# Performance work log

Hardware: AMD Instinct MI355X
Metric: run time of the kernel (lower is better)

Reference implementation:

```python
import jax, jax.numpy as jnp
import numpy as np

N, E, IN, OUT, T = 50000, 800000, 16, 16, 8
LN_EPS = 1e-5


def setup_inputs() -> dict:
    key = jax.random.key(0)
    ks = jax.random.split(key, 8)
    x = jax.random.normal(ks[0], (N, IN), dtype=jnp.float32)
    edge_index = jax.random.randint(ks[1], (2, E), 0, N, dtype=jnp.int64)
    edge_attr = jax.random.normal(ks[2], (E, T), dtype=jnp.float32)
    # LayerNorm params
    ln_gamma = jnp.ones((IN,), dtype=jnp.float32)
    ln_beta = jnp.zeros((IN,), dtype=jnp.float32)
    # edge_nn: Linear(t, in*out)
    w_edge = jax.random.normal(ks[3], (T, IN * OUT), dtype=jnp.float32) * (1.0 / np.sqrt(T))
    b_edge = jax.random.normal(ks[4], (IN * OUT,), dtype=jnp.float32) * 0.01
    # NNConv root weight [in, out] and bias [out]
    root = jax.random.normal(ks[5], (IN, OUT), dtype=jnp.float32) * (1.0 / np.sqrt(IN))
    bias = jax.random.normal(ks[6], (OUT,), dtype=jnp.float32) * 0.01
    return {"x": x, "edge_index": edge_index, "edge_attr": edge_attr,
            "ln_gamma": ln_gamma, "ln_beta": ln_beta,
            "w_edge": w_edge, "b_edge": b_edge, "root": root, "bias": bias}


def reference(x, edge_index, edge_attr, ln_gamma, ln_beta, w_edge, b_edge, root, bias):
    # pre: LayerNorm -> ReLU (Dropout is identity in eval mode)
    mu = jnp.mean(x, axis=-1, keepdims=True)
    var = jnp.mean((x - mu) ** 2, axis=-1, keepdims=True)
    h = (x - mu) * jax.lax.rsqrt(var + LN_EPS) * ln_gamma + ln_beta
    h = jax.nn.relu(h)  # [N, IN]

    # edge MLP -> per-edge weight matrices [E, IN, OUT]
    theta = (edge_attr @ w_edge + b_edge).reshape(E, IN, OUT)

    src = edge_index[0]  # message source j
    dst = edge_index[1]  # aggregation target i (PyG source_to_target flow)

    # per-edge matmul: x_j [E, IN] x theta [E, IN, OUT] -> [E, OUT]
    msg = jnp.einsum('ei,eio->eo', h[src], theta)

    # scatter-add into target nodes
    agg = jax.ops.segment_sum(msg, dst, num_segments=N)  # [N, OUT]

    # root transform + bias
    out = agg + h @ root + bias
    return out
```

## Files before the change

### kernel.cpp

```cpp
#include <hip/hip_runtime.h>

#define N_NODES 50000
#define E_EDGES 800000
#define NTILES  (E_EDGES / 16)

typedef __attribute__((ext_vector_type(8))) short short8;
typedef __attribute__((ext_vector_type(4))) float floatx4;

__device__ __forceinline__ short f2bf(float x) {
    union { float f; unsigned u; } v; v.f = x;
    unsigned r = v.u + 0x7FFFu + ((v.u >> 16) & 1u);
    return (short)(r >> 16);
}

__global__ __launch_bounds__(256) void node_kernel(
    const float* __restrict__ x, const float* __restrict__ gamma,
    const float* __restrict__ beta, const float* __restrict__ root,
    const float* __restrict__ bias, float* __restrict__ h,
    float* __restrict__ out)
{
    int n = blockIdx.x * blockDim.x + threadIdx.x;
    if (n >= N_NODES) return;
    const float* xr = x + n * 16;
    float xv[16];
    #pragma unroll
    for (int i = 0; i < 4; ++i) ((floatx4*)xv)[i] = ((const floatx4*)xr)[i];
    float mu = 0.f;
    #pragma unroll
    for (int i = 0; i < 16; ++i) mu += xv[i];
    mu *= (1.f / 16.f);
    float var = 0.f;
    #pragma unroll
    for (int i = 0; i < 16; ++i) { float d = xv[i] - mu; var += d * d; }
    var *= (1.f / 16.f);
    float rs = rsqrtf(var + 1e-5f);
    float hv[16];
    #pragma unroll
    for (int i = 0; i < 16; ++i) {
        float t = (xv[i] - mu) * rs * gamma[i] + beta[i];
        hv[i] = t > 0.f ? t : 0.f;
    }
    float* hr = h + n * 16;
    #pragma unroll
    for (int i = 0; i < 4; ++i) ((floatx4*)hr)[i] = ((floatx4*)hv)[i];
    float ov[16];
    #pragma unroll
    for (int o = 0; o < 16; ++o) ov[o] = bias[o];
    #pragma unroll
    for (int i = 0; i < 16; ++i) {
        float hi = hv[i];
        #pragma unroll
        for (int o = 0; o < 16; ++o) ov[o] += hi * root[i * 16 + o];
    }
    float* orow = out + n * 16;
    #pragma unroll
    for (int i = 0; i < 4; ++i) ((floatx4*)orow)[i] = ((floatx4*)ov)[i];
}

__global__ __launch_bounds__(256) void edge_kernel(
    const int* __restrict__ eidx, const float* __restrict__ ea,
    const float* __restrict__ w_edge, const float* __restrict__ b_edge,
    const float* __restrict__ h, float* __restrict__ out)
{
    const int lane = threadIdx.x & 63;
    const int wid  = threadIdx.x >> 6;
    const int m = lane & 15;
    const int q = lane >> 4;

    short8 bfrag[5];
    #pragma unroll
    for (int c = 0; c < 5; ++c) {
        short8 f;
        #pragma unroll
        for (int j = 0; j < 8; ++j) {
            int k = 32 * c + 8 * q + j;
            float v = 0.f;
            if (k < 128)      v = w_edge[(k >> 4) * 256 + (k & 15) * 16 + m];
            else if (k < 144) v = b_edge[(k - 128) * 16 + m];
            f[j] = f2bf(v);
        }
        bfrag[c] = f;
    }

    const int nw = (gridDim.x * blockDim.x) >> 6;
    for (int tile = blockIdx.x * (blockDim.x >> 6) + wid; tile < NTILES; tile += nw) {
        const int e   = tile * 16 + m;
        const int src = eidx[e];
        const int dst = eidx[E_EDGES + e];

        const float* er = ea + (size_t)e * 8;
        floatx4 ea0 = ((const floatx4*)er)[0];
        floatx4 ea1 = ((const floatx4*)er)[1];

        const float* hr = h + src * 16 + 8 * (q & 1);
        floatx4 h0 = ((const floatx4*)hr)[0];
        floatx4 h1 = ((const floatx4*)hr)[1];
        float hh[8] = {h0.x, h0.y, h0.z, h0.w, h1.x, h1.y, h1.z, h1.w};

        floatx4 acc = {0.f, 0.f, 0.f, 0.f};
        const int hi_t = q >> 1;
        #pragma unroll
        for (int c = 0; c < 4; ++c) {
            float t_even, t_odd;
            if (c == 0)      { t_even = ea0.x; t_odd = ea0.y; }
            else if (c == 1) { t_even = ea0.z; t_odd = ea0.w; }
            else if (c == 2) { t_even = ea1.x; t_odd = ea1.y; }
            else             { t_even = ea1.z; t_odd = ea1.w; }
            float s = hi_t ? t_odd : t_even;
            short8 af;
            #pragma unroll
            for (int j = 0; j < 8; ++j) af[j] = f2bf(s * hh[j]);
            acc = __builtin_amdgcn_mfma_f32_16x16x32_bf16(af, bfrag[c], acc, 0, 0, 0);
        }
        short8 af4;
        #pragma unroll
        for (int j = 0; j < 8; ++j) af4[j] = (q < 2) ? f2bf(hh[j]) : (short)0;
        acc = __builtin_amdgcn_mfma_f32_16x16x32_bf16(af4, bfrag[4], acc, 0, 0, 0);

        #pragma unroll
        for (int r = 0; r < 4; ++r) {
            int dr = __shfl(dst, 4 * q + r, 64);
            atomicAdd(out + (size_t)dr * 16 + m, acc[r]);
        }
    }
}

extern "C" void kernel_launch(void* const* d_in, const int* in_sizes, int n_in,
                              void* d_out, int out_size, void* d_ws, size_t ws_size,
                              hipStream_t stream) {
    const float* x        = (const float*)d_in[0];
    const int*   eidx     = (const int*)d_in[1];
    const float* ea       = (const float*)d_in[2];
    const float* ln_gamma = (const float*)d_in[3];
    const float* ln_beta  = (const float*)d_in[4];
    const float* w_edge   = (const float*)d_in[5];
    const float* b_edge   = (const float*)d_in[6];
    const float* root     = (const float*)d_in[7];
    const float* bias     = (const float*)d_in[8];
    float* out = (float*)d_out;
    float* h   = (float*)d_ws;

    node_kernel<<<(N_NODES + 255) / 256, 256, 0, stream>>>(
        x, ln_gamma, ln_beta, root, bias, h, out);
    edge_kernel<<<1024, 256, 0, stream>>>(eidx, ea, w_edge, b_edge, h, out);
}
```

Measured before the change: 133.7 us.

## Precompute bf16 edge weights, one tile per wave, pack bf16 via perm

Adds a prep kernel that converts the edge-MLP weights and bias into a transposed bf16 layout once, so each wave loads its MFMA B fragments with vector loads instead of gathering and converting them. The edge kernel drops its grid-stride loop and launches one wave per 16-edge tile, giving far more waves to hide gather and atomic latency. The bf16 conversion of activations now truncates through a byte permute rather than rounding to nearest even, which saves ALU work but changes numerics slightly. The cost is an extra kernel launch and a per-wave fragment reload from the small weight table.

Result: no change. 131.2 us (-1.9%).

```diff
diff --git a/kernel.cpp b/kernel.cpp
--- a/kernel.cpp
+++ b/kernel.cpp
@@ -11,6 +11,11 @@
     union { float f; unsigned u; } v; v.f = x;
     unsigned r = v.u + 0x7FFFu + ((v.u >> 16) & 1u);
     return (short)(r >> 16);
+}
+
+__device__ __forceinline__ unsigned pk_bf16(float lo, float hi) {
+    union { float f; unsigned u; } a, b; a.f = lo; b.f = hi;
+    return __builtin_amdgcn_perm(b.u, a.u, 0x07060302u);
 }
 
 __global__ __launch_bounds__(256) void node_kernel(
@@ -57,71 +62,80 @@
     for (int i = 0; i < 4; ++i) ((floatx4*)orow)[i] = ((floatx4*)ov)[i];
 }
 
+__global__ __launch_bounds__(256) void prep_kernel(
+    const float* __restrict__ w_edge, const float* __restrict__ b_edge,
+    short* __restrict__ w2t)
+{
+    int t = blockIdx.x * blockDim.x + threadIdx.x;
+    if (t >= 16 * 160) return;
+    int m = t / 160, k = t % 160;
+    float v = 0.f;
+    if (k < 128)      v = w_edge[(k >> 4) * 256 + (k & 15) * 16 + m];
+    else if (k < 144) v = b_edge[(k - 128) * 16 + m];
+    w2t[m * 160 + k] = f2bf(v);
+}
+
 __global__ __launch_bounds__(256) void edge_kernel(
     const int* __restrict__ eidx, const float* __restrict__ ea,
-    const float* __restrict__ w_edge, const float* __restrict__ b_edge,
-    const float* __restrict__ h, float* __restrict__ out)
+    const short* __restrict__ w2t, const float* __restrict__ h,
+    float* __restrict__ out)
 {
     const int lane = threadIdx.x & 63;
     const int wid  = threadIdx.x >> 6;
     const int m = lane & 15;
     const int q = lane >> 4;
 
+    const int tile = blockIdx.x * 4 + wid;
+    if (tile >= NTILES) return;
+
+    const int e   = tile * 16 + m;
+    const int src = eidx[e];
+    const int dst = eidx[E_EDGES + e];
+
+    const short* wp = w2t + m * 160 + 8 * q;
     short8 bfrag[5];
     #pragma unroll
-    for (int c = 0; c < 5; ++c) {
-        short8 f;
+    for (int c = 0; c < 5; ++c)
+        bfrag[c] = *(const short8*)(wp + 32 * c);
+
+    const float* er = ea + (size_t)e * 8;
+    floatx4 ea0 = ((const floatx4*)er)[0];
+    floatx4 ea1 = ((const floatx4*)er)[1];
+
+    const float* hr = h + src * 16 + 8 * (q & 1);
+    floatx4 h0 = ((const floatx4*)hr)[0];
+    floatx4 h1 = ((const floatx4*)hr)[1];
+    float hh[8] = {h0.x, h0.y, h0.z, h0.w, h1.x, h1.y, h1.z, h1.w};
+
+    floatx4 acc = {0.f, 0.f, 0.f, 0.f};
+    const int hi_t = q >> 1;
+    #pragma unroll
+    for (int c = 0; c < 4; ++c) {
+        float t_even, t_odd;
+        if (c == 0)      { t_even = ea0.x; t_odd = ea0.y; }
+        else if (c == 1) { t_even = ea0.z; t_odd = ea0.w; }
+        else if (c == 2) { t_even = ea1.x; t_odd = ea1.y; }
+        else             { t_even = ea1.z; t_odd = ea1.w; }
+        float s = hi_t ? t_odd : t_even;
+        union { short8 s8; unsigned u[4]; } af;
         #pragma unroll
-        for (int j = 0; j < 8; ++j) {
-            int k = 32 * c + 8 * q + j;
-            float v = 0.f;
-            if (k < 128)      v = w_edge[(k >> 4) * 256 + (k & 15) * 16 + m];
-            else if (k < 144) v = b_edge[(k - 128) * 16 + m];
-            f[j] = f2bf(v);
-        }
-        bfrag[c] = f;
+        for (int p = 0; p < 4; ++p)
+            af.u[p] = pk_bf16(s * hh[2 * p], s * hh[2 * p + 1]);
+        acc = __builtin_amdgcn_mfma_f32_16x16x32_bf16(af.s8, bfrag[c], acc, 0, 0, 0);
+    }
+    {
+        const unsigned msk = (q < 2) ? 0xFFFFFFFFu : 0u;
+        union { short8 s8; unsigned u[4]; } af;
+        #pragma unroll
+        for (int p = 0; p < 4; ++p)
+            af.u[p] = pk_bf16(hh[2 * p], hh[2 * p + 1]) & msk;
+        acc = __builtin_amdgcn_mfma_f32_16x16x32_bf16(af.s8, bfrag[4], acc, 0, 0, 0);
     }
 
-    const int nw = (gridDim.x * blockDim.x) >> 6;
-    for (int tile = blockIdx.x * (blockDim.x >> 6) + wid; tile < NTILES; tile += nw) {
-        const int e   = tile * 16 + m;
-        const int src = eidx[e];
-        const int dst = eidx[E_EDGES + e];
-
-        const float* er = ea + (size_t)e * 8;
-        floatx4 ea0 = ((const floatx4*)er)[0];
-        floatx4 ea1 = ((const floatx4*)er)[1];
-
-        const float* hr = h + src * 16 + 8 * (q & 1);
-        floatx4 h0 = ((const floatx4*)hr)[0];
-        floatx4 h1 = ((const floatx4*)hr)[1];
-        float hh[8] = {h0.x, h0.y, h0.z, h0.w, h1.x, h1.y, h1.z, h1.w};
-
-        floatx4 acc = {0.f, 0.f, 0.f, 0.f};
-        const int hi_t = q >> 1;
-        #pragma unroll
-        for (int c = 0; c < 4; ++c) {
-            float t_even, t_odd;
-            if (c == 0)      { t_even = ea0.x; t_odd = ea0.y; }
-            else if (c == 1) { t_even = ea0.z; t_odd = ea0.w; }
-            else if (c == 2) { t_even = ea1.x; t_odd = ea1.y; }
-            else             { t_even = ea1.z; t_odd = ea1.w; }
-            float s = hi_t ? t_odd : t_even;
-            short8 af;
-            #pragma unroll
-            for (int j = 0; j < 8; ++j) af[j] = f2bf(s * hh[j]);
-            acc = __builtin_amdgcn_mfma_f32_16x16x32_bf16(af, bfrag[c], acc, 0, 0, 0);
-        }
-        short8 af4;
-        #pragma unroll
-        for (int j = 0; j < 8; ++j) af4[j] = (q < 2) ? f2bf(hh[j]) : (short)0;
-        acc = __builtin_amdgcn_mfma_f32_16x16x32_bf16(af4, bfrag[4], acc, 0, 0, 0);
-
-        #pragma unroll
-        for (int r = 0; r < 4; ++r) {
-            int dr = __shfl(dst, 4 * q + r, 64);
-            atomicAdd(out + (size_t)dr * 16 + m, acc[r]);
-        }
+    #pragma unroll
+    for (int r = 0; r < 4; ++r) {
+        int dr = __shfl(dst, 4 * q + r, 64);
+        atomicAdd(out + (size_t)dr * 16 + m, acc[r]);
     }
 }
 
@@ -138,9 +152,13 @@
     const float* root     = (const float*)d_in[7];
     const float* bias     = (const float*)d_in[8];
     float* out = (float*)d_out;
-    float* h   = (float*)d_ws;
 
+    char* ws = (char*)d_ws;
+    float* h   = (float*)ws;
+    short* w2t = (short*)(ws + (size_t)N_NODES * 16 * 4);
+
+    prep_kernel<<<10, 256, 0, stream>>>(w_edge, b_edge, w2t);
     node_kernel<<<(N_NODES + 255) / 256, 256, 0, stream>>>(
         x, ln_gamma, ln_beta, root, bias, h, out);
-    edge_kernel<<<1024, 256, 0, stream>>>(eidx, ea, w_edge, b_edge, h, out);
+    edge_kernel<<<(NTILES + 3) / 4, 256, 0, stream>>>(eidx, ea, w2t, h, out);
 }
```
